# Performance work log

Measured on AMD Instinct MI355X. Metric: run time of the kernel, lower is better.

## Reference

```python
import jax, jax.numpy as jnp
import numpy as np
import math

B, S, HID, H = 2, 2048, 1024, 16
D = HID // H  # head_dim = 64

def _get_slopes(n):
    # power-of-2 branch (n=16)
    start = 2 ** (-2 ** (-(math.log2(n) - 3)))
    return np.array([start * 2 ** (-i) for i in range(n)], dtype=np.float32)

def setup_inputs() -> dict:
    key = jax.random.key(0)
    ks = jax.random.split(key, 9)
    sc = 1.0 / math.sqrt(HID)
    return {
        "x":  jax.random.normal(ks[0], (B, S, HID), dtype=jnp.float32),
        "Wq": jax.random.normal(ks[1], (HID, HID), dtype=jnp.float32) * sc,
        "bq": jnp.zeros((HID,), dtype=jnp.float32),
        "Wk": jax.random.normal(ks[2], (HID, HID), dtype=jnp.float32) * sc,
        "bk": jnp.zeros((HID,), dtype=jnp.float32),
        "Wv": jax.random.normal(ks[3], (HID, HID), dtype=jnp.float32) * sc,
        "bv": jnp.zeros((HID,), dtype=jnp.float32),
        "Wo": jax.random.normal(ks[4], (HID, HID), dtype=jnp.float32) * sc,
        "bo": jnp.zeros((HID,), dtype=jnp.float32),
        "slopes": jnp.asarray(_get_slopes(H)),
    }

def reference(x, Wq, bq, Wk, bk, Wv, bv, Wo, bo, slopes):
    b, s, hid = x.shape
    h = slopes.shape[0]
    d = hid // h
    # projections (torch Linear: y = x @ W.T + b), split heads -> [b,h,s,d]
    q = (x @ Wq.T + bq).reshape(b, s, h, d).transpose(0, 2, 1, 3)
    k = (x @ Wk.T + bk).reshape(b, s, h, d).transpose(0, 2, 1, 3)
    v = (x @ Wv.T + bv).reshape(b, s, h, d).transpose(0, 2, 1, 3)
    scores = jnp.einsum('bhqd,bhkd->bhqk', q, k) / jnp.sqrt(jnp.float32(d))
    # ALiBi bias: slope_h * (j - i), shape [h,s,s]
    pos = jnp.arange(s)
    dist = (pos[None, :] - pos[:, None]).astype(x.dtype)  # [s,s]
    scores = scores + slopes[None, :, None, None] * dist[None, None]
    attn = jax.nn.softmax(scores, axis=-1)
    ctx = jnp.einsum('bhqk,bhkd->bhqd', attn, v)
    ctx = ctx.transpose(0, 2, 1, 3).reshape(b, s, hid)
    return ctx @ Wo.T + bo
```

## Files before the change

### kernel.cpp

```cpp
#include <hip/hip_runtime.h>
#include <stdint.h>

typedef __attribute__((ext_vector_type(8))) short bf16x8;
typedef __attribute__((ext_vector_type(4))) short bf16x4;
typedef __attribute__((ext_vector_type(4))) float f32x4;
typedef unsigned short u16t;

#define DEVINL static __device__ __forceinline__

DEVINL u16t f2bf(float f) {
  union { float f; unsigned u; } v; v.f = f;
  return (u16t)((v.u + 0x7FFFu + ((v.u >> 16) & 1u)) >> 16);
}
DEVINL float bf2f(u16t u) {
  union { unsigned u; float f; } v; v.u = ((unsigned)u) << 16; return v.f;
}

DEVINL float exp2_fast(float x) {
  float r; asm("v_exp_f32 %0, %1" : "=v"(r) : "v"(x)); return r;
}
DEVINL unsigned cvt_pk_bf16(float a, float b) {
  unsigned r; asm("v_cvt_pk_bf16_f32 %0, %1, %2" : "=v"(r) : "v"(a), "v"(b)); return r;
}
DEVINL float max3f(float a, float b, float c) {
  float r; asm("v_max3_f32 %0, %1, %2, %3" : "=v"(r) : "v"(a), "v"(b), "v"(c)); return r;
}

DEVINL void gload16(const void* g, void* l) {
  __builtin_amdgcn_global_load_lds((const __attribute__((address_space(1))) void*)g,
                                   (__attribute__((address_space(3))) void*)l, 16, 0, 0);
}

__global__ __launch_bounds__(256)
void cvt5_kernel(const float* __restrict__ x, const float* __restrict__ wq,
                 const float* __restrict__ wk, const float* __restrict__ wv,
                 const float* __restrict__ wo, u16t* __restrict__ x_bf,
                 u16t* __restrict__ wqkv, u16t* __restrict__ wo_bf) {
  const int bid = blockIdx.x;
  const float* src; u16t* dst; int off;
  if (bid < 2048) { src = x; dst = x_bf; off = bid * 2048; }
  else {
    const int j = bid - 2048, sel = j >> 9;
    off = (j & 511) * 2048;
    if (sel == 0)      { src = wq; dst = wqkv; }
    else if (sel == 1) { src = wk; dst = wqkv + 1048576; }
    else if (sel == 2) { src = wv; dst = wqkv + 2097152; }
    else               { src = wo; dst = wo_bf; }
  }
  const int i = off + threadIdx.x * 8;
  float4 a = *(const float4*)(src + i);
  float4 b = *(const float4*)(src + i + 4);
  union { bf16x8 v; u16t u[8]; } o;
  o.u[0] = f2bf(a.x); o.u[1] = f2bf(a.y); o.u[2] = f2bf(a.z); o.u[3] = f2bf(a.w);
  o.u[4] = f2bf(b.x); o.u[5] = f2bf(b.y); o.u[6] = f2bf(b.z); o.u[7] = f2bf(b.w);
  *(bf16x8*)(dst + i) = o.v;
}

template <int MODE>
__global__ __launch_bounds__(256, 3)
void gemm_kernel(const u16t* __restrict__ A, const u16t* __restrict__ Bw,
                 const float* __restrict__ bias0, const float* __restrict__ bias1,
                 const float* __restrict__ bias2, void* __restrict__ outp) {
  __shared__ __attribute__((aligned(16))) u16t As[128 * 64];
  __shared__ __attribute__((aligned(16))) u16t Bs[128 * 64];
  const int tid = threadIdx.x;
  const int w = tid >> 6, l = tid & 63;
  const int wm = w >> 1, wn = w & 1;
  const int bm = blockIdx.x, bn = blockIdx.y;
  const int g = l >> 4, r16 = l & 15;
  const int srow = l >> 3, sslot = l & 7;

  f32x4 acc[4][4];
#pragma unroll
  for (int m = 0; m < 4; ++m)
#pragma unroll
    for (int n = 0; n < 4; ++n) acc[m][n] = f32x4{0.f, 0.f, 0.f, 0.f};

  const size_t arow0 = (size_t)bm * 128;
  const size_t brow0 = (size_t)bn * 128;

  for (int kt = 0; kt < 16; ++kt) {
    __syncthreads();
#pragma unroll
    for (int i = 0; i < 4; ++i) {
      const int row = (i * 4 + w) * 8 + srow;
      const int colA = kt * 64 + ((sslot ^ (row & 7)) * 8);
      gload16(A + (arow0 + row) * 1024 + colA, (char*)As + (i * 4 + w) * 1024);
      gload16(Bw + (brow0 + row) * 1024 + colA, (char*)Bs + (i * 4 + w) * 1024);
    }
    asm volatile("s_waitcnt vmcnt(0)" ::: "memory");
    __syncthreads();
#pragma unroll
    for (int kk = 0; kk < 2; ++kk) {
      bf16x8 af[4], bfr[4];
#pragma unroll
      for (int m = 0; m < 4; ++m) {
        const int rr = wm * 64 + m * 16 + r16;
        af[m] = *(const bf16x8*)((const char*)As + rr * 128 + (((kk * 4 + g) ^ (rr & 7)) * 16));
      }
#pragma unroll
      for (int n = 0; n < 4; ++n) {
        const int rr = wn * 64 + n * 16 + r16;
        bfr[n] = *(const bf16x8*)((const char*)Bs + rr * 128 + (((kk * 4 + g) ^ (rr & 7)) * 16));
      }
#pragma unroll
      for (int m = 0; m < 4; ++m)
#pragma unroll
        for (int n = 0; n < 4; ++n)
          acc[m][n] = __builtin_amdgcn_mfma_f32_16x16x32_bf16(af[m], bfr[n], acc[m][n], 0, 0, 0);
    }
  }

  if (MODE == 0) {
    const int mat = bn >> 3;
    if (mat == 2) {
      u16t* vt = (u16t*)outp + 8388608u;
#pragma unroll
      for (int n = 0; n < 4; ++n) {
        const int col = ((bn & 7) * 128) + wn * 64 + n * 16 + r16;
        const int hh = col >> 6, dd = col & 63;
        const float bv = bias2[col];
#pragma unroll
        for (int m = 0; m < 4; ++m) {
          const int row0 = bm * 128 + wm * 64 + m * 16 + g * 4;
          const int b_ = row0 >> 11, s_ = row0 & 2047;
          union { bf16x4 v; u16t u[4]; } o4;
#pragma unroll
          for (int i = 0; i < 4; ++i) o4.u[i] = f2bf(acc[m][n][i] + bv);
          *(bf16x4*)(vt + ((size_t)(b_ * 16 + hh) * 64 + dd) * 2048 + s_) = o4.v;
        }
      }
    } else {
      const float* bias = (mat == 0) ? bias0 : bias1;
      const float scale = (mat == 0) ? 0.18033688f : 1.0f;
      u16t* o = (u16t*)outp + (size_t)mat * 4194304u;
#pragma unroll
      for (int n = 0; n < 4; ++n) {
        const int col = ((bn & 7) * 128) + wn * 64 + n * 16 + r16;
        const float bv = bias[col];
#pragma unroll
        for (int m = 0; m < 4; ++m) {
          const int row = bm * 128 + wm * 64 + m * 16 + g * 4;
#pragma unroll
          for (int i = 0; i < 4; ++i)
            o[(size_t)(row + i) * 1024 + col] = f2bf((acc[m][n][i] + bv) * scale);
        }
      }
    }
  } else {
    float* o = (float*)outp;
#pragma unroll
    for (int n = 0; n < 4; ++n) {
      const int col = bn * 128 + wn * 64 + n * 16 + r16;
      const float bv = bias0[col];
#pragma unroll
      for (int m = 0; m < 4; ++m) {
        const int row = bm * 128 + wm * 64 + m * 16 + g * 4;
#pragma unroll
        for (int i = 0; i < 4; ++i)
          o[(size_t)(row + i) * 1024 + col] = acc[m][n][i] + bv;
      }
    }
  }
}

__global__ __launch_bounds__(256, 2)
void attn_kernel(const u16t* __restrict__ Qb, const u16t* __restrict__ Kb,
                 const u16t* __restrict__ Vtb, const float* __restrict__ slopes,
                 u16t* __restrict__ O0, u16t* __restrict__ O1,
                 float2* __restrict__ ML) {
  __shared__ __attribute__((aligned(16))) u16t Kl[3][2048];
  __shared__ __attribute__((aligned(16))) u16t Vl[2][2048];
  const int tid = threadIdx.x;
  const int w = tid >> 6, l = tid & 63;
  const int g = l >> 4, r = l & 15;
  const int qt = blockIdx.x;
  const int slot = blockIdx.y >> 1, b = blockIdx.y & 1;
  int h, sp;
  if (slot < 10)       { h = 6 + slot;  sp = 1; }
  else if (slot < 19)  { h = slot - 3;  sp = 0; }
  else if (slot == 19) { h = 5; sp = 1; }
  else if (slot == 20) { h = 6; sp = 0; }
  else if (slot < 26)  { h = 25 - slot; sp = 1; }
  else                 { h = slot - 26; sp = 0; }
  const float slope2 = slopes[h] * 1.44269504f;
  const int qpos = qt * 64 + w * 16 + r;
  const size_t base = (size_t)b * 2097152 + (size_t)h * 64;

  const float Wkeys = 26.0f / slope2;
  const int wt = (int)ceilf(Wkeys * 0.03125f);
  const int n = sp ? (wt < 32 ? wt : 32)
                   : (wt - 32 < 0 ? 0 : (wt - 32 < 32 ? wt - 32 : 32));
  if (n == 0) {
    if (l < 16)
      ML[((size_t)(sp * 2 + b) * 16 + h) * 2048 + qpos] = float2{-3.0e38f, 0.f};
    return;
  }

  const u16t* qrow = Qb + base + (size_t)qpos * 1024;
  const bf16x8 qf0 = *(const bf16x8*)(qrow + g * 8);
  const bf16x8 qf1 = *(const bf16x8*)(qrow + 32 + g * 8);
  asm volatile("s_waitcnt vmcnt(0)" ::: "memory");

  const int sig = 8 * (r >> 2) + (r & 3);
  const int toffs[2] = {0, 4};
  int koff[2][2], voff[4];
#pragma unroll
  for (int t = 0; t < 2; ++t) {
    const int row = toffs[t] + sig;
    const int mk = (row & 3) ^ ((row >> 1) & 4);
#pragma unroll
    for (int hh = 0; hh < 2; ++hh) koff[t][hh] = row * 128 + (((hh * 4 + g) ^ mk) * 16);
  }
#pragma unroll
  for (int db = 0; db < 4; ++db)
    voff[db] = (8 * db + (r >> 1)) * 128 + ((((((r & 1) << 2) | g)) ^ ((r >> 1) & 3)) * 16);

  const int kline_s = w * 8 + (l >> 3);
  const int ku_s = ((l & 7) ^ ((kline_s & 3) ^ ((kline_s >> 1) & 4))) * 8;
  const int vu_s = (l & 7) ^ (kline_s & 3);
  const int vd_s = 2 * kline_s + (vu_s >> 2);
  const int vcol_s = (vu_s & 3) * 8;

  f32x4 cv[2];
#pragma unroll
  for (int t = 0; t < 2; ++t)
#pragma unroll
    for (int i = 0; i < 4; ++i) cv[t][i] = slope2 * (float)(toffs[t] + 8 * g + i);

  const float d32 = slope2 * 32.f;
  float mj = -3.0e38f;
  f32x4 oc[4], sacc;
#pragma unroll
  for (int d = 0; d < 4; ++d) oc[d] = f32x4{0.f, 0.f, 0.f, 0.f};
  sacc = f32x4{0.f, 0.f, 0.f, 0.f};
  union { bf16x8 v; u16t u[8]; } ones;
#pragma unroll
  for (int i = 0; i < 8; ++i) ones.u[i] = 0x3F80;

  const u16t* Krow = Kb + base;
  const u16t* Vrow = Vtb + (size_t)(b * 16 + h) * 131072;
  const int kt0 = sp * 32 + 31;

#define STAGE_K(kt_, b_)                                                          \
  gload16(Krow + (size_t)((kt_) * 32 + kline_s) * 1024 + ku_s,                    \
          (char*)Kl + (b_) * 4096 + w * 1024);
#define STAGE_V(kt_, b_)                                                          \
  gload16(Vrow + (size_t)vd_s * 2048 + (kt_) * 32 + vcol_s,                       \
          (char*)Vl + (b_) * 4096 + w * 1024);

  const int ktp = (n > 1) ? kt0 - 1 : kt0;
  STAGE_K(kt0, 0)
  STAGE_V(kt0, 0)
  STAGE_K(ktp, 1)

  for (int it = 0; it < n; ++it) {
    const int kt = kt0 - it;
    const int kbuf = it % 3, vbuf = it & 1;
    if (it == n - 1) { asm volatile("s_waitcnt vmcnt(0)" ::: "memory"); }
    else             { asm volatile("s_waitcnt vmcnt(1)" ::: "memory"); }
    __builtin_amdgcn_s_barrier();
    asm volatile("" ::: "memory");
    if (it + 1 < n) STAGE_V(kt - 1, vbuf ^ 1)
    if (it + 2 < n) STAGE_K(kt - 2, (it + 2) % 3)
    if (it) mj += d32;

    const char* KB = (const char*)Kl + kbuf * 4096;
    const char* VB = (const char*)Vl + vbuf * 4096;

    f32x4 st[2];
    __builtin_amdgcn_s_setprio(1);
#pragma unroll
    for (int t = 0; t < 2; ++t) {
      st[t] = __builtin_amdgcn_mfma_f32_16x16x32_bf16(
          *(const bf16x8*)(KB + koff[t][0]), qf0, cv[t], 0, 0, 0);
      st[t] = __builtin_amdgcn_mfma_f32_16x16x32_bf16(
          *(const bf16x8*)(KB + koff[t][1]), qf1, st[t], 0, 0, 0);
    }
    __builtin_amdgcn_s_setprio(0);

    float pe[8];
#pragma unroll
    for (int t = 0; t < 2; ++t)
#pragma unroll
      for (int i = 0; i < 4; ++i) pe[t * 4 + i] = exp2_fast(st[t][i] - mj);

    const float m1 = max3f(st[0][0], st[0][1], st[0][2]);
    const float m2 = max3f(st[0][3], st[1][0], st[1][1]);
    const float m3 = max3f(st[1][2], st[1][3], m1);
    const float tm = fmaxf(m2, m3);
    if (__any(tm > mj)) {
      float tr = fmaxf(tm, __shfl_xor(tm, 16));
      tr = fmaxf(tr, __shfl_xor(tr, 32));
      const float mn = fmaxf(mj, tr);
      const float corr = exp2_fast(mj - mn);
#pragma unroll
      for (int d = 0; d < 4; ++d) {
        oc[d][0] *= corr; oc[d][1] *= corr; oc[d][2] *= corr; oc[d][3] *= corr;
      }
      sacc[0] *= corr; sacc[1] *= corr; sacc[2] *= corr; sacc[3] *= corr;
      mj = mn;
#pragma unroll
      for (int t = 0; t < 2; ++t)
#pragma unroll
        for (int i = 0; i < 4; ++i) pe[t * 4 + i] = exp2_fast(st[t][i] - mj);
    }

    union { bf16x8 v; unsigned q[4]; } pb;
#pragma unroll
    for (int j = 0; j < 4; ++j) pb.q[j] = cvt_pk_bf16(pe[j * 2], pe[j * 2 + 1]);

    __builtin_amdgcn_s_setprio(1);
#pragma unroll
    for (int db = 0; db < 4; ++db)
      oc[db] = __builtin_amdgcn_mfma_f32_16x16x32_bf16(
          *(const bf16x8*)(VB + voff[db]), pb.v, oc[db], 0, 0, 0);
    sacc = __builtin_amdgcn_mfma_f32_16x16x32_bf16(ones.v, pb.v, sacc, 0, 0, 0);
    __builtin_amdgcn_s_setprio(0);
  }
#undef STAGE_K
#undef STAGE_V

  u16t* op = (sp ? O1 : O0) + base + (size_t)qpos * 1024;
#pragma unroll
  for (int d = 0; d < 4; ++d) {
    union { bf16x4 v; u16t u[4]; } o4;
#pragma unroll
    for (int i = 0; i < 4; ++i) o4.u[i] = f2bf(oc[d][i]);
    *(bf16x4*)(op + d * 16 + g * 4) = o4.v;
  }
  if (l < 16) {
    const float m_global = mj + d32 * (float)(kt0 - n + 1);
    ML[((size_t)(sp * 2 + b) * 16 + h) * 2048 + qpos] = float2{m_global, sacc[0]};
  }
}

__global__ __launch_bounds__(256)
void combine_kernel(u16t* __restrict__ O0 ,
                    const u16t* __restrict__ O1, const float2* __restrict__ ML) {
  const int idx = blockIdx.x * 256 + threadIdx.x;
  const int colg = idx & 127, tok = idx >> 7;
  const int b = tok >> 11, s = tok & 2047, h = colg >> 3;
  const float2 ml0 = ML[((size_t)(0 + b) * 16 + h) * 2048 + s];
  const float2 ml1 = ML[((size_t)(2 + b) * 16 + h) * 2048 + s];
  const float M = fmaxf(ml0.x, ml1.x);
  const float e0 = exp2_fast(ml0.x - M), e1 = exp2_fast(ml1.x - M);
  const float invL = 1.f / (ml0.y * e0 + ml1.y * e1);
  const float w0 = e0 * invL, w1 = e1 * invL;
  union { bf16x8 v; u16t u[8]; } a, c, o;
  a.v = *(const bf16x8*)(O0 + (size_t)idx * 8);
  c.v = *(const bf16x8*)(O1 + (size_t)idx * 8);
#pragma unroll
  for (int i = 0; i < 8; ++i) o.u[i] = f2bf(bf2f(a.u[i]) * w0 + bf2f(c.u[i]) * w1);
  *(bf16x8*)(O0 + (size_t)idx * 8) = o.v;
}

extern "C" void kernel_launch(void* const* d_in, const int* in_sizes, int n_in,
                              void* d_out, int out_size, void* d_ws, size_t ws_size,
                              hipStream_t stream) {
  const float* x = (const float*)d_in[0];
  const float* Wq = (const float*)d_in[1];
  const float* bq = (const float*)d_in[2];
  const float* Wk = (const float*)d_in[3];
  const float* bk = (const float*)d_in[4];
  const float* Wv = (const float*)d_in[5];
  const float* bv = (const float*)d_in[6];
  const float* Wo = (const float*)d_in[7];
  const float* bo = (const float*)d_in[8];
  const float* slopes = (const float*)d_in[9];
  if (ws_size < (size_t)(48u << 20)) return;
  char* ws = (char*)d_ws;
  u16t* x_bf = (u16t*)(ws);
  u16t* wqkv = (u16t*)(ws + (8u << 20));
  u16t* wo_bf = (u16t*)(ws + (14u << 20));
  u16t* q_bf = (u16t*)(ws + (16u << 20));
  u16t* ctx_bf = (u16t*)(ws + (40u << 20));
  u16t* part1 = (u16t*)(ws);
  float2* ml = (float2*)(ws + (8u << 20));

  cvt5_kernel<<<4096, 256, 0, stream>>>(x, Wq, Wk, Wv, Wo, x_bf, wqkv, wo_bf);
  gemm_kernel<0><<<dim3(32, 24), 256, 0, stream>>>(x_bf, wqkv, bq, bk, bv, (void*)q_bf);
  attn_kernel<<<dim3(32, 64), 256, 0, stream>>>(q_bf, q_bf + 4194304, q_bf + 8388608,
                                                slopes, ctx_bf, part1, ml);
  combine_kernel<<<2048, 256, 0, stream>>>(ctx_bf, part1, ml);
  gemm_kernel<1><<<dim3(32, 8), 256, 0, stream>>>(ctx_bf, wo_bf, bo, bo, bo, d_out);
}
```

Measured before the change: 114.8 us.

## Process two query tiles per attention block to reuse staged K/V

```diff
diff --git a/kernel.cpp b/kernel.cpp
--- a/kernel.cpp
+++ b/kernel.cpp
@@ -184,22 +184,29 @@
   else if (slot < 26)  { h = 25 - slot; sp = 1; }
   else                 { h = slot - 26; sp = 0; }
   const float slope2 = slopes[h] * 1.44269504f;
-  const int qpos = qt * 64 + w * 16 + r;
+  const int qpos0 = qt * 128 + w * 16 + r;
+  const int qpos1 = qpos0 + 64;
   const size_t base = (size_t)b * 2097152 + (size_t)h * 64;
+  const size_t mlb = ((size_t)(sp * 2 + b) * 16 + h) * 2048;
 
   const float Wkeys = 26.0f / slope2;
   const int wt = (int)ceilf(Wkeys * 0.03125f);
   const int n = sp ? (wt < 32 ? wt : 32)
                    : (wt - 32 < 0 ? 0 : (wt - 32 < 32 ? wt - 32 : 32));
   if (n == 0) {
-    if (l < 16)
-      ML[((size_t)(sp * 2 + b) * 16 + h) * 2048 + qpos] = float2{-3.0e38f, 0.f};
+    if (l < 16) {
+      ML[mlb + qpos0] = float2{-3.0e38f, 0.f};
+      ML[mlb + qpos1] = float2{-3.0e38f, 0.f};
+    }
     return;
   }
 
-  const u16t* qrow = Qb + base + (size_t)qpos * 1024;
-  const bf16x8 qf0 = *(const bf16x8*)(qrow + g * 8);
-  const bf16x8 qf1 = *(const bf16x8*)(qrow + 32 + g * 8);
+  const u16t* qrow0 = Qb + base + (size_t)qpos0 * 1024;
+  const u16t* qrow1 = Qb + base + (size_t)qpos1 * 1024;
+  const bf16x8 qa0 = *(const bf16x8*)(qrow0 + g * 8);
+  const bf16x8 qa1 = *(const bf16x8*)(qrow0 + 32 + g * 8);
+  const bf16x8 qb0 = *(const bf16x8*)(qrow1 + g * 8);
+  const bf16x8 qb1 = *(const bf16x8*)(qrow1 + 32 + g * 8);
   asm volatile("s_waitcnt vmcnt(0)" ::: "memory");
 
   const int sig = 8 * (r >> 2) + (r & 3);
@@ -229,11 +236,15 @@
     for (int i = 0; i < 4; ++i) cv[t][i] = slope2 * (float)(toffs[t] + 8 * g + i);
 
   const float d32 = slope2 * 32.f;
-  float mj = -3.0e38f;
-  f32x4 oc[4], sacc;
-#pragma unroll
-  for (int d = 0; d < 4; ++d) oc[d] = f32x4{0.f, 0.f, 0.f, 0.f};
-  sacc = f32x4{0.f, 0.f, 0.f, 0.f};
+  float mjA = -3.0e38f, mjB = -3.0e38f;
+  f32x4 ocA[4], ocB[4], saccA, saccB;
+#pragma unroll
+  for (int d = 0; d < 4; ++d) {
+    ocA[d] = f32x4{0.f, 0.f, 0.f, 0.f};
+    ocB[d] = f32x4{0.f, 0.f, 0.f, 0.f};
+  }
+  saccA = f32x4{0.f, 0.f, 0.f, 0.f};
+  saccB = f32x4{0.f, 0.f, 0.f, 0.f};
   union { bf16x8 v; u16t u[8]; } ones;
 #pragma unroll
   for (int i = 0; i < 8; ++i) ones.u[i] = 0x3F80;
@@ -263,75 +274,100 @@
     asm volatile("" ::: "memory");
     if (it + 1 < n) STAGE_V(kt - 1, vbuf ^ 1)
     if (it + 2 < n) STAGE_K(kt - 2, (it + 2) % 3)
-    if (it) mj += d32;
+    if (it) { mjA += d32; mjB += d32; }
 
     const char* KB = (const char*)Kl + kbuf * 4096;
     const char* VB = (const char*)Vl + vbuf * 4096;
 
-    f32x4 st[2];
+    f32x4 stA[2], stB[2];
     __builtin_amdgcn_s_setprio(1);
 #pragma unroll
     for (int t = 0; t < 2; ++t) {
-      st[t] = __builtin_amdgcn_mfma_f32_16x16x32_bf16(
-          *(const bf16x8*)(KB + koff[t][0]), qf0, cv[t], 0, 0, 0);
-      st[t] = __builtin_amdgcn_mfma_f32_16x16x32_bf16(
-          *(const bf16x8*)(KB + koff[t][1]), qf1, st[t], 0, 0, 0);
+      const bf16x8 k0 = *(const bf16x8*)(KB + koff[t][0]);
+      const bf16x8 k1 = *(const bf16x8*)(KB + koff[t][1]);
+      stA[t] = __builtin_amdgcn_mfma_f32_16x16x32_bf16(k0, qa0, cv[t], 0, 0, 0);
+      stA[t] = __builtin_amdgcn_mfma_f32_16x16x32_bf16(k1, qa1, stA[t], 0, 0, 0);
+      stB[t] = __builtin_amdgcn_mfma_f32_16x16x32_bf16(k0, qb0, cv[t], 0, 0, 0);
+      stB[t] = __builtin_amdgcn_mfma_f32_16x16x32_bf16(k1, qb1, stB[t], 0, 0, 0);
     }
     __builtin_amdgcn_s_setprio(0);
 
-    float pe[8];
+    const float a1 = max3f(stA[0][0], stA[0][1], stA[0][2]);
+    const float a2 = max3f(stA[0][3], stA[1][0], stA[1][1]);
+    const float a3 = max3f(stA[1][2], stA[1][3], a1);
+    const float tmA = fmaxf(a2, a3);
+    const float b1 = max3f(stB[0][0], stB[0][1], stB[0][2]);
+    const float b2 = max3f(stB[0][3], stB[1][0], stB[1][1]);
+    const float b3 = max3f(stB[1][2], stB[1][3], b1);
+    const float tmB = fmaxf(b2, b3);
+    if (__any((tmA > mjA) || (tmB > mjB))) {
+      float trA = fmaxf(tmA, __shfl_xor(tmA, 16));
+      trA = fmaxf(trA, __shfl_xor(trA, 32));
+      const float mnA = fmaxf(mjA, trA);
+      const float corrA = exp2_fast(mjA - mnA);
+      float trB = fmaxf(tmB, __shfl_xor(tmB, 16));
+      trB = fmaxf(trB, __shfl_xor(trB, 32));
+      const float mnB = fmaxf(mjB, trB);
+      const float corrB = exp2_fast(mjB - mnB);
+#pragma unroll
+      for (int d = 0; d < 4; ++d)
+#pragma unroll
+        for (int i = 0; i < 4; ++i) {
+          ocA[d][i] *= corrA;
+          ocB[d][i] *= corrB;
+        }
+#pragma unroll
+      for (int i = 0; i < 4; ++i) { saccA[i] *= corrA; saccB[i] *= corrB; }
+      mjA = mnA; mjB = mnB;
+    }
+
+    float peA[8], peB[8];
 #pragma unroll
     for (int t = 0; t < 2; ++t)
 #pragma unroll
-      for (int i = 0; i < 4; ++i) pe[t * 4 + i] = exp2_fast(st[t][i] - mj);
-
-    const float m1 = max3f(st[0][0], st[0][1], st[0][2]);
-    const float m2 = max3f(st[0][3], st[1][0], st[1][1]);
-    const float m3 = max3f(st[1][2], st[1][3], m1);
-    const float tm = fmaxf(m2, m3);
-    if (__any(tm > mj)) {
-      float tr = fmaxf(tm, __shfl_xor(tm, 16));
-      tr = fmaxf(tr, __shfl_xor(tr, 32));
-      const float mn = fmaxf(mj, tr);
-      const float corr = exp2_fast(mj - mn);
-#pragma unroll
-      for (int d = 0; d < 4; ++d) {
-        oc[d][0] *= corr; oc[d][1] *= corr; oc[d][2] *= corr; oc[d][3] *= corr;
-      }
-      sacc[0] *= corr; sacc[1] *= corr; sacc[2] *= corr; sacc[3] *= corr;
-      mj = mn;
-#pragma unroll
-      for (int t = 0; t < 2; ++t)
-#pragma unroll
-        for (int i = 0; i < 4; ++i) pe[t * 4 + i] = exp2_fast(st[t][i] - mj);
-    }
-
-    union { bf16x8 v; unsigned q[4]; } pb;
-#pragma unroll
-    for (int j = 0; j < 4; ++j) pb.q[j] = cvt_pk_bf16(pe[j * 2], pe[j * 2 + 1]);
+      for (int i = 0; i < 4; ++i) {
+        peA[t * 4 + i] = exp2_fast(stA[t][i] - mjA);
+        peB[t * 4 + i] = exp2_fast(stB[t][i] - mjB);
+      }
+    union { bf16x8 v; unsigned q[4]; } pbA, pbB;
+#pragma unroll
+    for (int j = 0; j < 4; ++j) {
+      pbA.q[j] = cvt_pk_bf16(peA[j * 2], peA[j * 2 + 1]);
+      pbB.q[j] = cvt_pk_bf16(peB[j * 2], peB[j * 2 + 1]);
+    }
 
     __builtin_amdgcn_s_setprio(1);
 #pragma unroll
-    for (int db = 0; db < 4; ++db)
-      oc[db] = __builtin_amdgcn_mfma_f32_16x16x32_bf16(
-          *(const bf16x8*)(VB + voff[db]), pb.v, oc[db], 0, 0, 0);
-    sacc = __builtin_amdgcn_mfma_f32_16x16x32_bf16(ones.v, pb.v, sacc, 0, 0, 0);
+    for (int db = 0; db < 4; ++db) {
+      const bf16x8 vf = *(const bf16x8*)(VB + voff[db]);
+      ocA[db] = __builtin_amdgcn_mfma_f32_16x16x32_bf16(vf, pbA.v, ocA[db], 0, 0, 0);
+      ocB[db] = __builtin_amdgcn_mfma_f32_16x16x32_bf16(vf, pbB.v, ocB[db], 0, 0, 0);
+    }
+    saccA = __builtin_amdgcn_mfma_f32_16x16x32_bf16(ones.v, pbA.v, saccA, 0, 0, 0);
+    saccB = __builtin_amdgcn_mfma_f32_16x16x32_bf16(ones.v, pbB.v, saccB, 0, 0, 0);
     __builtin_amdgcn_s_setprio(0);
   }
 #undef STAGE_K
 #undef STAGE_V
 
-  u16t* op = (sp ? O1 : O0) + base + (size_t)qpos * 1024;
+  u16t* opbase = (sp ? O1 : O0) + base;
+  u16t* op0 = opbase + (size_t)qpos0 * 1024;
+  u16t* op1 = opbase + (size_t)qpos1 * 1024;
 #pragma unroll
   for (int d = 0; d < 4; ++d) {
-    union { bf16x4 v; u16t u[4]; } o4;
-#pragma unroll
-    for (int i = 0; i < 4; ++i) o4.u[i] = f2bf(oc[d][i]);
-    *(bf16x4*)(op + d * 16 + g * 4) = o4.v;
+    union { bf16x4 v; u16t u[4]; } oa, ob;
+#pragma unroll
+    for (int i = 0; i < 4; ++i) {
+      oa.u[i] = f2bf(ocA[d][i]);
+      ob.u[i] = f2bf(ocB[d][i]);
+    }
+    *(bf16x4*)(op0 + d * 16 + g * 4) = oa.v;
+    *(bf16x4*)(op1 + d * 16 + g * 4) = ob.v;
   }
   if (l < 16) {
-    const float m_global = mj + d32 * (float)(kt0 - n + 1);
-    ML[((size_t)(sp * 2 + b) * 16 + h) * 2048 + qpos] = float2{m_global, sacc[0]};
+    const float mshift = d32 * (float)(kt0 - n + 1);
+    ML[mlb + qpos0] = float2{mjA + mshift, saccA[0]};
+    ML[mlb + qpos1] = float2{mjB + mshift, saccB[0]};
   }
 }
 
@@ -380,7 +416,7 @@
 
   cvt5_kernel<<<4096, 256, 0, stream>>>(x, Wq, Wk, Wv, Wo, x_bf, wqkv, wo_bf);
   gemm_kernel<0><<<dim3(32, 24), 256, 0, stream>>>(x_bf, wqkv, bq, bk, bv, (void*)q_bf);
-  attn_kernel<<<dim3(32, 64), 256, 0, stream>>>(q_bf, q_bf + 4194304, q_bf + 8388608,
+  attn_kernel<<<dim3(16, 64), 256, 0, stream>>>(q_bf, q_bf + 4194304, q_bf + 8388608,
                                                 slopes, ctx_bf, part1, ml);
   combine_kernel<<<2048, 256, 0, stream>>>(ctx_bf, part1, ml);
   gemm_kernel<1><<<dim3(32, 8), 256, 0, stream>>>(ctx_bf, wo_bf, bo, bo, bo, d_out);
```

Result: no change. 115.0 us (+0.2%).

## Fuse split-KV combine into output projection GEMM A-tile load

Applied to the files above, without the earlier changes.

```diff
diff --git a/kernel.cpp b/kernel.cpp
--- a/kernel.cpp
+++ b/kernel.cpp
@@ -56,7 +56,6 @@
   *(bf16x8*)(dst + i) = o.v;
 }
 
-template <int MODE>
 __global__ __launch_bounds__(256, 3)
 void gemm_kernel(const u16t* __restrict__ A, const u16t* __restrict__ Bw,
                  const float* __restrict__ bias0, const float* __restrict__ bias1,
@@ -111,55 +110,126 @@
     }
   }
 
-  if (MODE == 0) {
-    const int mat = bn >> 3;
-    if (mat == 2) {
-      u16t* vt = (u16t*)outp + 8388608u;
-#pragma unroll
-      for (int n = 0; n < 4; ++n) {
-        const int col = ((bn & 7) * 128) + wn * 64 + n * 16 + r16;
-        const int hh = col >> 6, dd = col & 63;
-        const float bv = bias2[col];
-#pragma unroll
-        for (int m = 0; m < 4; ++m) {
-          const int row0 = bm * 128 + wm * 64 + m * 16 + g * 4;
-          const int b_ = row0 >> 11, s_ = row0 & 2047;
-          union { bf16x4 v; u16t u[4]; } o4;
-#pragma unroll
-          for (int i = 0; i < 4; ++i) o4.u[i] = f2bf(acc[m][n][i] + bv);
-          *(bf16x4*)(vt + ((size_t)(b_ * 16 + hh) * 64 + dd) * 2048 + s_) = o4.v;
-        }
-      }
-    } else {
-      const float* bias = (mat == 0) ? bias0 : bias1;
-      const float scale = (mat == 0) ? 0.18033688f : 1.0f;
-      u16t* o = (u16t*)outp + (size_t)mat * 4194304u;
-#pragma unroll
-      for (int n = 0; n < 4; ++n) {
-        const int col = ((bn & 7) * 128) + wn * 64 + n * 16 + r16;
-        const float bv = bias[col];
-#pragma unroll
-        for (int m = 0; m < 4; ++m) {
-          const int row = bm * 128 + wm * 64 + m * 16 + g * 4;
-#pragma unroll
-          for (int i = 0; i < 4; ++i)
-            o[(size_t)(row + i) * 1024 + col] = f2bf((acc[m][n][i] + bv) * scale);
-        }
+  const int mat = bn >> 3;
+  if (mat == 2) {
+    u16t* vt = (u16t*)outp + 8388608u;
+#pragma unroll
+    for (int n = 0; n < 4; ++n) {
+      const int col = ((bn & 7) * 128) + wn * 64 + n * 16 + r16;
+      const int hh = col >> 6, dd = col & 63;
+      const float bv = bias2[col];
+#pragma unroll
+      for (int m = 0; m < 4; ++m) {
+        const int row0 = bm * 128 + wm * 64 + m * 16 + g * 4;
+        const int b_ = row0 >> 11, s_ = row0 & 2047;
+        union { bf16x4 v; u16t u[4]; } o4;
+#pragma unroll
+        for (int i = 0; i < 4; ++i) o4.u[i] = f2bf(acc[m][n][i] + bv);
+        *(bf16x4*)(vt + ((size_t)(b_ * 16 + hh) * 64 + dd) * 2048 + s_) = o4.v;
       }
     }
   } else {
-    float* o = (float*)outp;
+    const float* bias = (mat == 0) ? bias0 : bias1;
+    const float scale = (mat == 0) ? 0.18033688f : 1.0f;
+    u16t* o = (u16t*)outp + (size_t)mat * 4194304u;
 #pragma unroll
     for (int n = 0; n < 4; ++n) {
-      const int col = bn * 128 + wn * 64 + n * 16 + r16;
-      const float bv = bias0[col];
+      const int col = ((bn & 7) * 128) + wn * 64 + n * 16 + r16;
+      const float bv = bias[col];
 #pragma unroll
       for (int m = 0; m < 4; ++m) {
         const int row = bm * 128 + wm * 64 + m * 16 + g * 4;
 #pragma unroll
         for (int i = 0; i < 4; ++i)
-          o[(size_t)(row + i) * 1024 + col] = acc[m][n][i] + bv;
-      }
+          o[(size_t)(row + i) * 1024 + col] = f2bf((acc[m][n][i] + bv) * scale);
+      }
+    }
+  }
+}
+
+__global__ __launch_bounds__(256, 3)
+void gemm1_fused(const u16t* __restrict__ O0, const u16t* __restrict__ O1,
+                 const float2* __restrict__ ML, const u16t* __restrict__ Bw,
+                 const float* __restrict__ bias, float* __restrict__ outp) {
+  __shared__ __attribute__((aligned(16))) u16t As[128 * 64];
+  __shared__ __attribute__((aligned(16))) u16t Bs[128 * 64];
+  const int tid = threadIdx.x;
+  const int w = tid >> 6, l = tid & 63;
+  const int wm = w >> 1, wn = w & 1;
+  const int bm = blockIdx.x, bn = blockIdx.y;
+  const int g = l >> 4, r16 = l & 15;
+  const int srow = l >> 3, sslot = l & 7;
+
+  f32x4 acc[4][4];
+#pragma unroll
+  for (int m = 0; m < 4; ++m)
+#pragma unroll
+    for (int n = 0; n < 4; ++n) acc[m][n] = f32x4{0.f, 0.f, 0.f, 0.f};
+
+  const size_t arow0 = (size_t)bm * 128;
+  const size_t brow0 = (size_t)bn * 128;
+
+  for (int kt = 0; kt < 16; ++kt) {
+    __syncthreads();
+#pragma unroll
+    for (int i = 0; i < 4; ++i) {
+      const int row = (i * 4 + w) * 8 + srow;
+      const int colB = kt * 64 + ((sslot ^ (row & 7)) * 8);
+      gload16(Bw + (brow0 + row) * 1024 + colB, (char*)Bs + (i * 4 + w) * 1024);
+    }
+#pragma unroll
+    for (int i = 0; i < 4; ++i) {
+      const int row = (i * 4 + w) * 8 + srow;
+      const size_t grow = arow0 + row;
+      const int c0 = kt * 64 + ((sslot ^ (row & 7)) * 8);
+      const int b_ = (int)(grow >> 11), s_ = (int)(grow & 2047);
+      const float2 ml0 = ML[((size_t)b_ * 16 + kt) * 2048 + s_];
+      const float2 ml1 = ML[((size_t)(2 + b_) * 16 + kt) * 2048 + s_];
+      const float M = fmaxf(ml0.x, ml1.x);
+      const float e0 = exp2_fast(ml0.x - M), e1 = exp2_fast(ml1.x - M);
+      const float invL = 1.f / (ml0.y * e0 + ml1.y * e1);
+      const float w0 = e0 * invL, w1 = e1 * invL;
+      union { bf16x8 v; u16t u[8]; } a0, a1, pk;
+      a0.v = *(const bf16x8*)(O0 + grow * 1024 + c0);
+      a1.v = *(const bf16x8*)(O1 + grow * 1024 + c0);
+#pragma unroll
+      for (int e = 0; e < 8; ++e)
+        pk.u[e] = f2bf(bf2f(a0.u[e]) * w0 + bf2f(a1.u[e]) * w1);
+      *(bf16x8*)(As + (i * 4 + w) * 512 + l * 8) = pk.v;
+    }
+    asm volatile("s_waitcnt vmcnt(0)" ::: "memory");
+    __syncthreads();
+#pragma unroll
+    for (int kk = 0; kk < 2; ++kk) {
+      bf16x8 af[4], bfr[4];
+#pragma unroll
+      for (int m = 0; m < 4; ++m) {
+        const int rr = wm * 64 + m * 16 + r16;
+        af[m] = *(const bf16x8*)((const char*)As + rr * 128 + (((kk * 4 + g) ^ (rr & 7)) * 16));
+      }
+#pragma unroll
+      for (int n = 0; n < 4; ++n) {
+        const int rr = wn * 64 + n * 16 + r16;
+        bfr[n] = *(const bf16x8*)((const char*)Bs + rr * 128 + (((kk * 4 + g) ^ (rr & 7)) * 16));
+      }
+#pragma unroll
+      for (int m = 0; m < 4; ++m)
+#pragma unroll
+        for (int n = 0; n < 4; ++n)
+          acc[m][n] = __builtin_amdgcn_mfma_f32_16x16x32_bf16(af[m], bfr[n], acc[m][n], 0, 0, 0);
+    }
+  }
+
+#pragma unroll
+  for (int n = 0; n < 4; ++n) {
+    const int col = bn * 128 + wn * 64 + n * 16 + r16;
+    const float bv = bias[col];
+#pragma unroll
+    for (int m = 0; m < 4; ++m) {
+      const int row = bm * 128 + wm * 64 + m * 16 + g * 4;
+#pragma unroll
+      for (int i = 0; i < 4; ++i)
+        outp[(size_t)(row + i) * 1024 + col] = acc[m][n][i] + bv;
     }
   }
 }
@@ -279,12 +349,6 @@
     }
     __builtin_amdgcn_s_setprio(0);
 
-    float pe[8];
-#pragma unroll
-    for (int t = 0; t < 2; ++t)
-#pragma unroll
-      for (int i = 0; i < 4; ++i) pe[t * 4 + i] = exp2_fast(st[t][i] - mj);
-
     const float m1 = max3f(st[0][0], st[0][1], st[0][2]);
     const float m2 = max3f(st[0][3], st[1][0], st[1][1]);
     const float m3 = max3f(st[1][2], st[1][3], m1);
@@ -300,12 +364,13 @@
       }
       sacc[0] *= corr; sacc[1] *= corr; sacc[2] *= corr; sacc[3] *= corr;
       mj = mn;
-#pragma unroll
-      for (int t = 0; t < 2; ++t)
-#pragma unroll
-        for (int i = 0; i < 4; ++i) pe[t * 4 + i] = exp2_fast(st[t][i] - mj);
-    }
-
+    }
+
+    float pe[8];
+#pragma unroll
+    for (int t = 0; t < 2; ++t)
+#pragma unroll
+      for (int i = 0; i < 4; ++i) pe[t * 4 + i] = exp2_fast(st[t][i] - mj);
     union { bf16x8 v; unsigned q[4]; } pb;
 #pragma unroll
     for (int j = 0; j < 4; ++j) pb.q[j] = cvt_pk_bf16(pe[j * 2], pe[j * 2 + 1]);
@@ -333,26 +398,6 @@
     const float m_global = mj + d32 * (float)(kt0 - n + 1);
     ML[((size_t)(sp * 2 + b) * 16 + h) * 2048 + qpos] = float2{m_global, sacc[0]};
   }
-}
-
-__global__ __launch_bounds__(256)
-void combine_kernel(u16t* __restrict__ O0 ,
-                    const u16t* __restrict__ O1, const float2* __restrict__ ML) {
-  const int idx = blockIdx.x * 256 + threadIdx.x;
-  const int colg = idx & 127, tok = idx >> 7;
-  const int b = tok >> 11, s = tok & 2047, h = colg >> 3;
-  const float2 ml0 = ML[((size_t)(0 + b) * 16 + h) * 2048 + s];
-  const float2 ml1 = ML[((size_t)(2 + b) * 16 + h) * 2048 + s];
-  const float M = fmaxf(ml0.x, ml1.x);
-  const float e0 = exp2_fast(ml0.x - M), e1 = exp2_fast(ml1.x - M);
-  const float invL = 1.f / (ml0.y * e0 + ml1.y * e1);
-  const float w0 = e0 * invL, w1 = e1 * invL;
-  union { bf16x8 v; u16t u[8]; } a, c, o;
-  a.v = *(const bf16x8*)(O0 + (size_t)idx * 8);
-  c.v = *(const bf16x8*)(O1 + (size_t)idx * 8);
-#pragma unroll
-  for (int i = 0; i < 8; ++i) o.u[i] = f2bf(bf2f(a.u[i]) * w0 + bf2f(c.u[i]) * w1);
-  *(bf16x8*)(O0 + (size_t)idx * 8) = o.v;
 }
 
 extern "C" void kernel_launch(void* const* d_in, const int* in_sizes, int n_in,
@@ -374,14 +419,14 @@
   u16t* wqkv = (u16t*)(ws + (8u << 20));
   u16t* wo_bf = (u16t*)(ws + (14u << 20));
   u16t* q_bf = (u16t*)(ws + (16u << 20));
-  u16t* ctx_bf = (u16t*)(ws + (40u << 20));
+  u16t* part0 = (u16t*)(ws + (40u << 20));
   u16t* part1 = (u16t*)(ws);
   float2* ml = (float2*)(ws + (8u << 20));
 
   cvt5_kernel<<<4096, 256, 0, stream>>>(x, Wq, Wk, Wv, Wo, x_bf, wqkv, wo_bf);
-  gemm_kernel<0><<<dim3(32, 24), 256, 0, stream>>>(x_bf, wqkv, bq, bk, bv, (void*)q_bf);
+  gemm_kernel<<<dim3(32, 24), 256, 0, stream>>>(x_bf, wqkv, bq, bk, bv, (void*)q_bf);
   attn_kernel<<<dim3(32, 64), 256, 0, stream>>>(q_bf, q_bf + 4194304, q_bf + 8388608,
-                                                slopes, ctx_bf, part1, ml);
-  combine_kernel<<<2048, 256, 0, stream>>>(ctx_bf, part1, ml);
-  gemm_kernel<1><<<dim3(32, 8), 256, 0, stream>>>(ctx_bf, wo_bf, bo, bo, bo, d_out);
-}
+                                                slopes, part0, part1, ml);
+  gemm1_fused<<<dim3(32, 8), 256, 0, stream>>>(part0, part1, ml, wo_bf, bo,
+                                               (float*)d_out);
+}
```

Measured after the change: 147.1 us. 1.28x slower.
